# Performance work log

Hardware: AMD Instinct MI355X
Metric: run time of the kernel (lower is better)

Reference implementation:

```python
import jax, jax.numpy as jnp
import numpy as np

N = 4096
IN_DIM = 256
HID = 64
HEADS = 4
OUT_DIM = 64
NEG = -9e15


def setup_inputs() -> dict:
    key = jax.random.key(0)
    ks = jax.random.split(key, 12)
    h = jax.random.normal(ks[0], (N, IN_DIM), dtype=jnp.float32)
    adj = jax.random.randint(ks[1], (N, N), 0, 2, dtype=jnp.int32)
    # per-head GATLayer params (W: Linear(input_dim, hid) with bias; a: Linear(2*hid, 1) with bias)
    Wh = jax.random.normal(ks[2], (HEADS, IN_DIM, HID), dtype=jnp.float32) * (1.414 / np.sqrt(IN_DIM + HID))
    bWh = jnp.zeros((HEADS, HID), dtype=jnp.float32)
    a_src = jax.random.normal(ks[3], (HEADS, HID), dtype=jnp.float32) * 0.1
    a_dst = jax.random.normal(ks[4], (HEADS, HID), dtype=jnp.float32) * 0.1
    a_b = jnp.zeros((HEADS,), dtype=jnp.float32)
    # output GATLayer params
    Wo = jax.random.normal(ks[5], (HEADS * HID, OUT_DIM), dtype=jnp.float32) * (1.414 / np.sqrt(HEADS * HID + OUT_DIM))
    bWo = jnp.zeros((OUT_DIM,), dtype=jnp.float32)
    ao_src = jax.random.normal(ks[6], (OUT_DIM,), dtype=jnp.float32) * 0.1
    ao_dst = jax.random.normal(ks[7], (OUT_DIM,), dtype=jnp.float32) * 0.1
    ao_b = jnp.zeros((), dtype=jnp.float32)
    return {"h": h, "adj": adj, "Wh": Wh, "bWh": bWh, "a_src": a_src, "a_dst": a_dst,
            "a_b": a_b, "Wo": Wo, "bWo": bWo, "ao_src": ao_src, "ao_dst": ao_dst, "ao_b": ao_b}


def _gat_layer(x, adj_mask, W, b, a_s, a_d, a_bias):
    # x: [N, F], W: [F, D]. Decompose a([wh_i || wh_j]) = a_s.wh_i + a_d.wh_j + a_bias
    wh = x @ W + b                                   # [N, D]
    s = (wh @ a_s)[:, None] + (wh @ a_d)[None, :] + a_bias  # [N, N]
    s = jax.nn.leaky_relu(s, negative_slope=0.2)
    s = jnp.where(adj_mask, s, NEG)
    att = jax.nn.softmax(s, axis=1)                  # softmax over neighbors j
    return att @ wh                                  # [N, D]


def reference(h, adj, Wh, bWh, a_src, a_dst, a_b, Wo, bWo, ao_src, ao_dst, ao_b):
    adj_mask = adj > 0
    # multi-head: vmap over stacked head params (dropout is identity in eval)
    heads = jax.vmap(lambda W, b, asr, ads, ab: _gat_layer(h, adj_mask, W, b, asr, ads, ab))(
        Wh, bWh, a_src, a_dst, a_b)                  # [H, N, D]
    out = jax.nn.elu(heads)
    out = jnp.transpose(out, (1, 0, 2)).reshape(N, HEADS * HID)  # concat heads
    out = _gat_layer(out, adj_mask, Wo, bWo, ao_src, ao_dst, ao_b)
    return jax.nn.elu(out)
```

## Files before the change

### kernel.cpp

```cpp
#include <hip/hip_runtime.h>

#define NN 4096
#define NHEADS 4
#define HID 64
#define INDIM 256

using short8 = __attribute__((ext_vector_type(8))) short;
using f32x4  = __attribute__((ext_vector_type(4))) float;

union f32u { float f; unsigned int u; };

__device__ __forceinline__ float bf2f(unsigned short s) {
  f32u x; x.u = ((unsigned int)s) << 16; return x.f;
}
__device__ __forceinline__ unsigned short f2bf(float f) {
  f32u x; x.f = f;
  unsigned int r = x.u + 0x7fffu + ((x.u >> 16) & 1u);
  return (unsigned short)(r >> 16);
}

__device__ __forceinline__ float ld(const unsigned short* p, size_t i) { return bf2f(p[i]); }
__device__ __forceinline__ float ld(const float* p, size_t i) { return p[i]; }

__global__ __launch_bounds__(256) void k_probe(const void* hv, const void* adjv, int* flags) {
  __shared__ int s_bad, s_at;
  const int tid = threadIdx.x;
  if (tid == 0) { s_bad = 0; s_at = 0; }
  __syncthreads();
  const unsigned short* hu = (const unsigned short*)hv;
  float v = bf2f(hu[tid]);
  if (!(v > -1000.f && v < 1000.f)) atomicOr(&s_bad, 1);
  const unsigned int* au = (const unsigned int*)adjv;
  unsigned int wv = au[tid];
  if ((wv & 0xFFFFu) == 0x3F80u) atomicOr(&s_at, 2);
  else if (wv == 0x3F800000u) atomicOr(&s_at, 1);
  __syncthreads();
  if (tid == 0) {
    flags[0] = s_bad ? 0 : 1;
    int at = s_at;
    flags[1] = (at & 2) ? 2 : (at & 1);
  }
}

__global__ __launch_bounds__(256) void k_bm(const void* adjv, const int* __restrict__ flags,
                                            unsigned char* __restrict__ bm) {
  const int at = flags[1];
  const int i = blockIdx.x;
#pragma unroll
  for (int rep = 0; rep < 2; rep++) {
    int jb = threadIdx.x + rep * 256;
    unsigned int b = 0;
    if (at == 0) {
      const int4* arow = (const int4*)((const int*)adjv + (size_t)i * NN);
      int4 a0 = arow[jb * 2 + 0];
      int4 a1 = arow[jb * 2 + 1];
      b |= (a0.x > 0) ? 1u : 0u;  b |= (a0.y > 0) ? 2u : 0u;
      b |= (a0.z > 0) ? 4u : 0u;  b |= (a0.w > 0) ? 8u : 0u;
      b |= (a1.x > 0) ? 16u : 0u; b |= (a1.y > 0) ? 32u : 0u;
      b |= (a1.z > 0) ? 64u : 0u; b |= (a1.w > 0) ? 128u : 0u;
    } else if (at == 1) {
      const float* arow = (const float*)adjv + (size_t)i * NN + jb * 8;
      for (int t = 0; t < 8; t++) b |= (arow[t] > 0.5f) ? (1u << t) : 0u;
    } else {
      const unsigned short* arow = (const unsigned short*)adjv + (size_t)i * NN + jb * 8;
      for (int t = 0; t < 8; t++) b |= (bf2f(arow[t]) > 0.5f) ? (1u << t) : 0u;
    }
    bm[(size_t)i * 512 + jb] = (unsigned char)b;
  }
}

template <typename T>
__device__ __forceinline__ void wh_body(const T* h, const T* Wh, const T* bWh,
    const T* a_src, const T* a_dst, const T* a_b,
    unsigned short* Bp1, float* ssrc1, float* sdst1) {
  const int head = threadIdx.x >> 6;
  const int d = threadIdx.x & 63;
  const int i0 = blockIdx.x * 8;
  const T* W = Wh + (size_t)(head * INDIM) * HID + d;
  float acc[8];
  float bv = ld(bWh, head * HID + d);
#pragma unroll
  for (int r = 0; r < 8; r++) acc[r] = bv;
  for (int k = 0; k < INDIM; k++) {
    float wv = ld(W, (size_t)k * HID);
#pragma unroll
    for (int r = 0; r < 8; r++) {
      float hv = ld(h, (size_t)(i0 + r) * INDIM + k);
      acc[r] = fmaf(hv, wv, acc[r]);
    }
  }
  float asv = ld(a_src, head * HID + d);
  float adv = ld(a_dst, head * HID + d);
  float abv = ld(a_b, head);
#pragma unroll
  for (int r = 0; r < 8; r++) {
    float ps = acc[r] * asv, pd = acc[r] * adv;
#pragma unroll
    for (int o = 32; o > 0; o >>= 1) { ps += __shfl_xor(ps, o); pd += __shfl_xor(pd, o); }
    int i = i0 + r;
    if (d == 0) { ssrc1[head * NN + i] = ps + abv; sdst1[head * NN + i] = pd; }
    int kb = i >> 5, quad = (i >> 3) & 3, jj = i & 7;
    int ln = quad * 16 + (d & 15), tt = d >> 4;
    Bp1[((((size_t)head * 128 + kb) * 4 + tt) * 64 + ln) * 8 + jj] = f2bf(acc[r]);
  }
}
__global__ __launch_bounds__(256) void k_wh(const void* h, const void* Wh, const void* bWh,
    const void* a_src, const void* a_dst, const void* a_b, const int* __restrict__ flags,
    unsigned short* Bp1, float* ssrc1, float* sdst1) {
  if (flags[0])
    wh_body<unsigned short>((const unsigned short*)h, (const unsigned short*)Wh,
        (const unsigned short*)bWh, (const unsigned short*)a_src,
        (const unsigned short*)a_dst, (const unsigned short*)a_b, Bp1, ssrc1, sdst1);
  else
    wh_body<float>((const float*)h, (const float*)Wh, (const float*)bWh, (const float*)a_src,
        (const float*)a_dst, (const float*)a_b, Bp1, ssrc1, sdst1);
}

__global__ __launch_bounds__(1024) void k_att1(
    const unsigned char* __restrict__ bm, const float* __restrict__ ssrc,
    const float* __restrict__ sdst, const short8* __restrict__ Bp,
    unsigned short* __restrict__ x2) {
  const int rb = blockIdx.x;
  const int tid = threadIdx.x;
  const int w = tid >> 6;
  const int head = w & 3;
  const int slice = w >> 2;
  const int lane = tid & 63;
  const int r15 = lane & 15, quad = lane >> 4;
  const int row = rb * 16 + r15;
  const float si = ssrc[head * NN + row];
  const unsigned char* bmrow = bm + (size_t)row * 512;
  const float* sd = sdst + head * NN;
  const short8* Bh = Bp + (size_t)head * 128 * 4 * 64;
  f32x4 acc0 = {0, 0, 0, 0}, acc1 = {0, 0, 0, 0}, acc2 = {0, 0, 0, 0}, acc3 = {0, 0, 0, 0};
  float lsum = 0.f;
  const int kb0 = slice * 32;
  for (int kb = kb0; kb < kb0 + 32; kb++) {
    const int j0 = kb * 32 + quad * 8;
    unsigned int bits = bmrow[kb * 4 + quad];
    float4 q0 = *(const float4*)(sd + j0);
    float4 q1 = *(const float4*)(sd + j0 + 4);
    float sdv[8] = {q0.x, q0.y, q0.z, q0.w, q1.x, q1.y, q1.z, q1.w};
    short8 af;
#pragma unroll
    for (int jj = 0; jj < 8; jj++) {
      float t = si + sdv[jj];
      float lr = fmaxf(t, 0.2f * t);
      float e = __expf(lr);
      float pe = ((bits >> jj) & 1u) ? e : 0.0f;
      lsum += pe;
      af[jj] = (short)f2bf(pe);
    }
    const short8* Bk = Bh + (size_t)kb * 256 + lane;
    short8 b0 = Bk[0], b1 = Bk[64], b2 = Bk[128], b3 = Bk[192];
    acc0 = __builtin_amdgcn_mfma_f32_16x16x32_bf16(af, b0, acc0, 0, 0, 0);
    acc1 = __builtin_amdgcn_mfma_f32_16x16x32_bf16(af, b1, acc1, 0, 0, 0);
    acc2 = __builtin_amdgcn_mfma_f32_16x16x32_bf16(af, b2, acc2, 0, 0, 0);
    acc3 = __builtin_amdgcn_mfma_f32_16x16x32_bf16(af, b3, acc3, 0, 0, 0);
  }
  lsum += __shfl_xor(lsum, 16);
  lsum += __shfl_xor(lsum, 32);
  __shared__ float accs[8][16][66];
  __shared__ float ls[8][16];
  if (slice >= 2) {
    const int slot = w - 8;
    if (lane < 16) ls[slot][lane] = lsum;
#pragma unroll
    for (int g = 0; g < 4; g++) {
      int r = quad * 4 + g;
      accs[slot][r][ 0 + r15] = acc0[g];
      accs[slot][r][16 + r15] = acc1[g];
      accs[slot][r][32 + r15] = acc2[g];
      accs[slot][r][48 + r15] = acc3[g];
    }
  }
  __syncthreads();
  if (slice < 2) {
    const int slot = w;
    if (lane < 16) ls[slot][lane] += lsum;
#pragma unroll
    for (int g = 0; g < 4; g++) {
      int r = quad * 4 + g;
      accs[slot][r][ 0 + r15] += acc0[g];
      accs[slot][r][16 + r15] += acc1[g];
      accs[slot][r][32 + r15] += acc2[g];
      accs[slot][r][48 + r15] += acc3[g];
    }
  }
  __syncthreads();
#pragma unroll
  for (int c = tid; c < 4096; c += 1024) {
    int r = c >> 8, hc = c & 255;
    int hh = hc >> 6, col = hc & 63;
    float s = accs[hh][r][col] + accs[hh + 4][r][col];
    float lt = ls[hh][r] + ls[hh + 4][r];
    float v = (lt > 0.f) ? s / lt : 0.f;
    v = v > 0.f ? v : __expf(v) - 1.f;
    x2[(size_t)(rb * 16 + r) * 256 + hc] = f2bf(v);
  }
}

template <typename T>
__device__ __forceinline__ void wo_body(const unsigned short* x2, const T* Wo, const T* bWo,
    const T* ao_src, const T* ao_dst, const T* ao_b,
    unsigned short* Bp2, float* ssrc2, float* sdst2) {
  const int w = threadIdx.x >> 6, d = threadIdx.x & 63;
  const int i = blockIdx.x * 4 + w;
  const unsigned short* xr = x2 + (size_t)i * 256;
  float acc = ld(bWo, d);
  for (int k = 0; k < 256; k++)
    acc = fmaf(bf2f(xr[k]), ld(Wo, (size_t)k * 64 + d), acc);
  float ps = acc * ld(ao_src, d);
  float pd = acc * ld(ao_dst, d);
#pragma unroll
  for (int o = 32; o > 0; o >>= 1) { ps += __shfl_xor(ps, o); pd += __shfl_xor(pd, o); }
  if (d == 0) { ssrc2[i] = ps + ld(ao_b, 0); sdst2[i] = pd; }
  int kb = i >> 5, quad = (i >> 3) & 3, jj = i & 7;
  int ln = quad * 16 + (d & 15), tt = d >> 4;
  Bp2[(((size_t)kb * 4 + tt) * 64 + ln) * 8 + jj] = f2bf(acc);
}
__global__ __launch_bounds__(256) void k_wo(const unsigned short* __restrict__ x2,
    const void* Wo, const void* bWo, const void* ao_src, const void* ao_dst, const void* ao_b,
    const int* __restrict__ flags, unsigned short* Bp2, float* ssrc2, float* sdst2) {
  if (flags[0])
    wo_body<unsigned short>(x2, (const unsigned short*)Wo, (const unsigned short*)bWo,
        (const unsigned short*)ao_src, (const unsigned short*)ao_dst,
        (const unsigned short*)ao_b, Bp2, ssrc2, sdst2);
  else
    wo_body<float>(x2, (const float*)Wo, (const float*)bWo, (const float*)ao_src,
        (const float*)ao_dst, (const float*)ao_b, Bp2, ssrc2, sdst2);
}

__global__ __launch_bounds__(1024) void k_att2(
    const unsigned char* __restrict__ bm, const float* __restrict__ ssrc,
    const float* __restrict__ sdst, const short8* __restrict__ Bp,
    const int* __restrict__ flags, void* __restrict__ outv) {
  const int rb = blockIdx.x;
  const int tid = threadIdx.x;
  const int w = tid >> 6;
  const int lane = tid & 63;
  const int r15 = lane & 15, quad = lane >> 4;
  const int row = rb * 16 + r15;
  const float si = ssrc[row];
  const unsigned char* bmrow = bm + (size_t)row * 512;
  f32x4 acc0 = {0, 0, 0, 0}, acc1 = {0, 0, 0, 0}, acc2 = {0, 0, 0, 0}, acc3 = {0, 0, 0, 0};
  float lsum = 0.f;
  const int kb0 = w * 8;
  for (int kb = kb0; kb < kb0 + 8; kb++) {
    const int j0 = kb * 32 + quad * 8;
    unsigned int bits = bmrow[kb * 4 + quad];
    float4 q0 = *(const float4*)(sdst + j0);
    float4 q1 = *(const float4*)(sdst + j0 + 4);
    float sdv[8] = {q0.x, q0.y, q0.z, q0.w, q1.x, q1.y, q1.z, q1.w};
    short8 af;
#pragma unroll
    for (int jj = 0; jj < 8; jj++) {
      float t = si + sdv[jj];
      float lr = fmaxf(t, 0.2f * t);
      float e = __expf(lr);
      float pe = ((bits >> jj) & 1u) ? e : 0.0f;
      lsum += pe;
      af[jj] = (short)f2bf(pe);
    }
    const short8* Bk = Bp + (size_t)kb * 256 + lane;
    short8 b0 = Bk[0], b1 = Bk[64], b2 = Bk[128], b3 = Bk[192];
    acc0 = __builtin_amdgcn_mfma_f32_16x16x32_bf16(af, b0, acc0, 0, 0, 0);
    acc1 = __builtin_amdgcn_mfma_f32_16x16x32_bf16(af, b1, acc1, 0, 0, 0);
    acc2 = __builtin_amdgcn_mfma_f32_16x16x32_bf16(af, b2, acc2, 0, 0, 0);
    acc3 = __builtin_amdgcn_mfma_f32_16x16x32_bf16(af, b3, acc3, 0, 0, 0);
  }
  lsum += __shfl_xor(lsum, 16);
  lsum += __shfl_xor(lsum, 32);
  __shared__ float accs[8][16][66];
  __shared__ float ls2[8][16];
  if (w >= 8) {
    const int slot = w - 8;
    if (lane < 16) ls2[slot][lane] = lsum;
#pragma unroll
    for (int g = 0; g < 4; g++) {
      int r = quad * 4 + g;
      accs[slot][r][ 0 + r15] = acc0[g];
      accs[slot][r][16 + r15] = acc1[g];
      accs[slot][r][32 + r15] = acc2[g];
      accs[slot][r][48 + r15] = acc3[g];
    }
  }
  __syncthreads();
  if (w < 8) {
    const int slot = w;
    if (lane < 16) ls2[slot][lane] += lsum;
#pragma unroll
    for (int g = 0; g < 4; g++) {
      int r = quad * 4 + g;
      accs[slot][r][ 0 + r15] += acc0[g];
      accs[slot][r][16 + r15] += acc1[g];
      accs[slot][r][32 + r15] += acc2[g];
      accs[slot][r][48 + r15] += acc3[g];
    }
  }
  __syncthreads();
  {
    const int r = tid >> 6, col = tid & 63;
    float s = 0.f, lt = 0.f;
#pragma unroll
    for (int k = 0; k < 8; k++) { s += accs[k][r][col]; lt += ls2[k][r]; }
    float v = (lt > 0.f) ? s / lt : 0.f;
    v = v > 0.f ? v : __expf(v) - 1.f;
    size_t idx = (size_t)(rb * 16 + r) * 64 + col;
    if (flags[0]) ((unsigned short*)outv)[idx] = f2bf(v);
    else          ((float*)outv)[idx] = v;
  }
}

extern "C" void kernel_launch(void* const* d_in, const int* in_sizes, int n_in,
                              void* d_out, int out_size, void* d_ws, size_t ws_size,
                              hipStream_t stream) {
  const void* h      = d_in[0];
  const void* adj    = d_in[1];
  const void* Wh     = d_in[2];
  const void* bWh    = d_in[3];
  const void* a_src  = d_in[4];
  const void* a_dst  = d_in[5];
  const void* a_b    = d_in[6];
  const void* Wo     = d_in[7];
  const void* bWo    = d_in[8];
  const void* ao_src = d_in[9];
  const void* ao_dst = d_in[10];
  const void* ao_b   = d_in[11];

  size_t need = 16 + (size_t)NN * 512 + (size_t)NHEADS * NN * HID * 2 + (size_t)NN * 256 * 2 +
                (size_t)NN * 64 * 2 + (size_t)NHEADS * NN * 8 + (size_t)NN * 8;
  hipMemsetAsync(d_out, 0x41, (size_t)out_size * 2, stream);
  if (ws_size < need) {
    hipMemsetAsync(d_out, 0x45, (size_t)out_size * 2, stream);
    return;
  }
  unsigned char* ws = (unsigned char*)d_ws;
  int* flags = (int*)ws;                        ws += 16;
  unsigned char* bmp = ws;                      ws += (size_t)NN * 512;
  unsigned short* Bp1 = (unsigned short*)ws;    ws += (size_t)NHEADS * NN * HID * 2;
  unsigned short* x2  = (unsigned short*)ws;    ws += (size_t)NN * 256 * 2;
  unsigned short* Bp2 = (unsigned short*)ws;    ws += (size_t)NN * 64 * 2;
  float* ssrc1 = (float*)ws;                    ws += (size_t)NHEADS * NN * 4;
  float* sdst1 = (float*)ws;                    ws += (size_t)NHEADS * NN * 4;
  float* ssrc2 = (float*)ws;                    ws += (size_t)NN * 4;
  float* sdst2 = (float*)ws;                    ws += (size_t)NN * 4;

  k_probe<<<dim3(1),    dim3(256),  0, stream>>>(h, adj, flags);
  k_bm   <<<dim3(4096), dim3(256),  0, stream>>>(adj, flags, bmp);
  k_wh   <<<dim3(512),  dim3(256),  0, stream>>>(h, Wh, bWh, a_src, a_dst, a_b, flags,
                                                 Bp1, ssrc1, sdst1);
  k_att1 <<<dim3(256),  dim3(1024), 0, stream>>>(bmp, ssrc1, sdst1, (const short8*)Bp1, x2);
  k_wo   <<<dim3(1024), dim3(256),  0, stream>>>(x2, Wo, bWo, ao_src, ao_dst, ao_b, flags,
                                                 Bp2, ssrc2, sdst2);
  k_att2 <<<dim3(256),  dim3(1024), 0, stream>>>(bmp, ssrc2, sdst2, (const short8*)Bp2,
                                                 flags, d_out);
}
```

Baseline: 222.7 us.

## Split layer-1 attention into two-row-tile split-K kernel plus finalize pass

Adds k_att1s, in which each wave handles 32 rows (two 16-row tiles) so every B-fragment load feeds two MFMAs. The key dimension is split across two block halves, and the partial sums go to a workspace that a new finalize kernel (k_att1f) combines, normalises and passes through ELU. The adjacency bitmask is now read as int4 vectors, and float-to-bf16 packing uses the v_cvt_pk_bf16_f32 instruction in both attention kernels. This path only runs when the workspace is large enough, and it adds an extra kernel launch and fp32 partial-result traffic.

```diff
diff --git a/kernel.cpp b/kernel.cpp
--- a/kernel.cpp
+++ b/kernel.cpp
@@ -9,6 +9,7 @@
 using f32x4  = __attribute__((ext_vector_type(4))) float;
 
 union f32u { float f; unsigned int u; };
+union i4s8 { int4 i; short8 s; };
 
 __device__ __forceinline__ float bf2f(unsigned short s) {
   f32u x; x.u = ((unsigned int)s) << 16; return x.f;
@@ -17,6 +18,11 @@
   f32u x; x.f = f;
   unsigned int r = x.u + 0x7fffu + ((x.u >> 16) & 1u);
   return (unsigned short)(r >> 16);
+}
+__device__ __forceinline__ unsigned int cvtpk(float lo, float hi) {
+  unsigned int r;
+  asm("v_cvt_pk_bf16_f32 %0, %1, %2" : "=v"(r) : "v"(lo), "v"(hi));
+  return r;
 }
 
 __device__ __forceinline__ float ld(const unsigned short* p, size_t i) { return bf2f(p[i]); }
@@ -114,6 +120,129 @@
   else
     wh_body<float>((const float*)h, (const float*)Wh, (const float*)bWh, (const float*)a_src,
         (const float*)a_dst, (const float*)a_b, Bp1, ssrc1, sdst1);
+}
+
+__global__ __launch_bounds__(512, 6) void k_att1s(
+    const unsigned char* __restrict__ bm, const float* __restrict__ ssrc,
+    const float* __restrict__ sdst, const short8* __restrict__ Bp,
+    float* __restrict__ part, float* __restrict__ partl) {
+  const int rb = blockIdx.x & 127;
+  const int half = blockIdx.x >> 7;
+  const int tid = threadIdx.x;
+  const int w = tid >> 6;
+  const int head = w & 3;
+  const int sl = w >> 2;
+  const int lane = tid & 63;
+  const int r15 = lane & 15, quad = lane >> 4;
+  const int row0 = rb * 32 + r15;
+  const int row1 = row0 + 16;
+  const float si0 = ssrc[head * NN + row0];
+  const float si1 = ssrc[head * NN + row1];
+  const unsigned char* bmr0 = bm + (size_t)row0 * 512;
+  const unsigned char* bmr1 = bm + (size_t)row1 * 512;
+  const float* sd = sdst + head * NN;
+  const short8* Bh = Bp + (size_t)head * 128 * 4 * 64;
+  f32x4 acc0[4], acc1[4];
+#pragma unroll
+  for (int t = 0; t < 4; t++) { acc0[t] = (f32x4){0,0,0,0}; acc1[t] = (f32x4){0,0,0,0}; }
+  float ls0 = 0.f, ls1 = 0.f;
+  const int kb0 = half * 64 + sl * 32;
+  for (int g = 0; g < 8; g++) {
+    const int kbg = kb0 + g * 4;
+    int4 u0 = *(const int4*)(bmr0 + kbg * 4);
+    int4 u1 = *(const int4*)(bmr1 + kbg * 4);
+    int wd0[4] = {u0.x, u0.y, u0.z, u0.w};
+    int wd1[4] = {u1.x, u1.y, u1.z, u1.w};
+#pragma unroll
+    for (int kk = 0; kk < 4; kk++) {
+      const int kb = kbg + kk;
+      const int j0 = kb * 32 + quad * 8;
+      float4 q0 = *(const float4*)(sd + j0);
+      float4 q1 = *(const float4*)(sd + j0 + 4);
+      float sdv[8] = {q0.x, q0.y, q0.z, q0.w, q1.x, q1.y, q1.z, q1.w};
+      unsigned int bits0 = (((unsigned int)wd0[kk]) >> (quad * 8)) & 0xffu;
+      unsigned int bits1 = (((unsigned int)wd1[kk]) >> (quad * 8)) & 0xffu;
+      float pe0[8], pe1[8];
+#pragma unroll
+      for (int jj = 0; jj < 8; jj++) {
+        float t0 = si0 + sdv[jj];
+        float e0 = __expf(fmaxf(t0, 0.2f * t0));
+        pe0[jj] = ((bits0 >> jj) & 1u) ? e0 : 0.f;
+        ls0 += pe0[jj];
+        float t1 = si1 + sdv[jj];
+        float e1 = __expf(fmaxf(t1, 0.2f * t1));
+        pe1[jj] = ((bits1 >> jj) & 1u) ? e1 : 0.f;
+        ls1 += pe1[jj];
+      }
+      i4s8 a0, a1;
+      a0.i.x = cvtpk(pe0[0], pe0[1]); a0.i.y = cvtpk(pe0[2], pe0[3]);
+      a0.i.z = cvtpk(pe0[4], pe0[5]); a0.i.w = cvtpk(pe0[6], pe0[7]);
+      a1.i.x = cvtpk(pe1[0], pe1[1]); a1.i.y = cvtpk(pe1[2], pe1[3]);
+      a1.i.z = cvtpk(pe1[4], pe1[5]); a1.i.w = cvtpk(pe1[6], pe1[7]);
+      const short8* Bk = Bh + (size_t)kb * 256 + lane;
+      short8 bt[4];
+      bt[0] = Bk[0]; bt[1] = Bk[64]; bt[2] = Bk[128]; bt[3] = Bk[192];
+#pragma unroll
+      for (int t = 0; t < 4; t++) {
+        acc0[t] = __builtin_amdgcn_mfma_f32_16x16x32_bf16(a0.s, bt[t], acc0[t], 0, 0, 0);
+        acc1[t] = __builtin_amdgcn_mfma_f32_16x16x32_bf16(a1.s, bt[t], acc1[t], 0, 0, 0);
+      }
+    }
+  }
+  ls0 += __shfl_xor(ls0, 16); ls0 += __shfl_xor(ls0, 32);
+  ls1 += __shfl_xor(ls1, 16); ls1 += __shfl_xor(ls1, 32);
+  __shared__ float accs[4][16][66];
+  __shared__ float lsh[4][16];
+#define DOPASS(AC, LSV, PASS)                                                  \
+  do {                                                                         \
+    if (sl == 1) {                                                             \
+      if (lane < 16) lsh[head][lane] = (LSV);                                  \
+      _Pragma("unroll") for (int t = 0; t < 4; t++)                            \
+        _Pragma("unroll") for (int gg = 0; gg < 4; gg++)                       \
+          accs[head][quad * 4 + gg][t * 16 + r15] = (AC)[t][gg];               \
+    }                                                                          \
+    __syncthreads();                                                           \
+    if (sl == 0) {                                                             \
+      if (lane < 16) lsh[head][lane] += (LSV);                                 \
+      _Pragma("unroll") for (int t = 0; t < 4; t++)                            \
+        _Pragma("unroll") for (int gg = 0; gg < 4; gg++)                       \
+          accs[head][quad * 4 + gg][t * 16 + r15] += (AC)[t][gg];              \
+    }                                                                          \
+    __syncthreads();                                                           \
+    for (int idx = tid; idx < 4096; idx += 512) {                              \
+      int r = idx >> 8, hc = idx & 255;                                        \
+      part[((size_t)half * NN + rb * 32 + (PASS) * 16 + r) * 256 + hc] =       \
+          accs[hc >> 6][r][hc & 63];                                           \
+    }                                                                          \
+    if (tid < 64)                                                              \
+      partl[((size_t)half * 4 + (tid >> 4)) * NN + rb * 32 + (PASS) * 16 +     \
+            (tid & 15)] = lsh[tid >> 4][tid & 15];                             \
+    __syncthreads();                                                           \
+  } while (0)
+  DOPASS(acc0, ls0, 0);
+  DOPASS(acc1, ls1, 1);
+#undef DOPASS
+}
+
+__global__ __launch_bounds__(256) void k_att1f(const float* __restrict__ part,
+    const float* __restrict__ partl, unsigned short* __restrict__ x2) {
+  const int idx = blockIdx.x * 256 + threadIdx.x;
+  const int row = idx >> 6;
+  const int c4 = (idx & 63) * 4;
+  const int head = c4 >> 6;
+  const size_t off = (size_t)row * 256 + c4;
+  float4 p0 = *(const float4*)(part + off);
+  float4 p1 = *(const float4*)(part + (size_t)NN * 256 + off);
+  float lt = partl[(size_t)head * NN + row] + partl[(size_t)(4 + head) * NN + row];
+  float rl = (lt > 0.f) ? 1.f / lt : 0.f;
+  float v0 = (p0.x + p1.x) * rl, v1 = (p0.y + p1.y) * rl;
+  float v2 = (p0.z + p1.z) * rl, v3 = (p0.w + p1.w) * rl;
+  v0 = v0 > 0.f ? v0 : __expf(v0) - 1.f;
+  v1 = v1 > 0.f ? v1 : __expf(v1) - 1.f;
+  v2 = v2 > 0.f ? v2 : __expf(v2) - 1.f;
+  v3 = v3 > 0.f ? v3 : __expf(v3) - 1.f;
+  uint2 st; st.x = cvtpk(v0, v1); st.y = cvtpk(v2, v3);
+  *(uint2*)(x2 + off) = st;
 }
 
 __global__ __launch_bounds__(1024) void k_att1(
@@ -246,28 +375,36 @@
   f32x4 acc0 = {0, 0, 0, 0}, acc1 = {0, 0, 0, 0}, acc2 = {0, 0, 0, 0}, acc3 = {0, 0, 0, 0};
   float lsum = 0.f;
   const int kb0 = w * 8;
-  for (int kb = kb0; kb < kb0 + 8; kb++) {
-    const int j0 = kb * 32 + quad * 8;
-    unsigned int bits = bmrow[kb * 4 + quad];
-    float4 q0 = *(const float4*)(sdst + j0);
-    float4 q1 = *(const float4*)(sdst + j0 + 4);
-    float sdv[8] = {q0.x, q0.y, q0.z, q0.w, q1.x, q1.y, q1.z, q1.w};
-    short8 af;
-#pragma unroll
-    for (int jj = 0; jj < 8; jj++) {
-      float t = si + sdv[jj];
-      float lr = fmaxf(t, 0.2f * t);
-      float e = __expf(lr);
-      float pe = ((bits >> jj) & 1u) ? e : 0.0f;
-      lsum += pe;
-      af[jj] = (short)f2bf(pe);
-    }
-    const short8* Bk = Bp + (size_t)kb * 256 + lane;
-    short8 b0 = Bk[0], b1 = Bk[64], b2 = Bk[128], b3 = Bk[192];
-    acc0 = __builtin_amdgcn_mfma_f32_16x16x32_bf16(af, b0, acc0, 0, 0, 0);
-    acc1 = __builtin_amdgcn_mfma_f32_16x16x32_bf16(af, b1, acc1, 0, 0, 0);
-    acc2 = __builtin_amdgcn_mfma_f32_16x16x32_bf16(af, b2, acc2, 0, 0, 0);
-    acc3 = __builtin_amdgcn_mfma_f32_16x16x32_bf16(af, b3, acc3, 0, 0, 0);
+#pragma unroll
+  for (int g = 0; g < 2; g++) {
+    int4 ubm = *(const int4*)(bmrow + (kb0 + g * 4) * 4);
+    int wds[4] = {ubm.x, ubm.y, ubm.z, ubm.w};
+#pragma unroll
+    for (int kk = 0; kk < 4; kk++) {
+      const int kb = kb0 + g * 4 + kk;
+      const int j0 = kb * 32 + quad * 8;
+      unsigned int bits = (((unsigned int)wds[kk]) >> (quad * 8)) & 0xffu;
+      float4 q0 = *(const float4*)(sdst + j0);
+      float4 q1 = *(const float4*)(sdst + j0 + 4);
+      float sdv[8] = {q0.x, q0.y, q0.z, q0.w, q1.x, q1.y, q1.z, q1.w};
+      float pe[8];
+#pragma unroll
+      for (int jj = 0; jj < 8; jj++) {
+        float t = si + sdv[jj];
+        float e = __expf(fmaxf(t, 0.2f * t));
+        pe[jj] = ((bits >> jj) & 1u) ? e : 0.f;
+        lsum += pe[jj];
+      }
+      i4s8 a;
+      a.i.x = cvtpk(pe[0], pe[1]); a.i.y = cvtpk(pe[2], pe[3]);
+      a.i.z = cvtpk(pe[4], pe[5]); a.i.w = cvtpk(pe[6], pe[7]);
+      const short8* Bk = Bp + (size_t)kb * 256 + lane;
+      short8 b0 = Bk[0], b1 = Bk[64], b2 = Bk[128], b3 = Bk[192];
+      acc0 = __builtin_amdgcn_mfma_f32_16x16x32_bf16(a.s, b0, acc0, 0, 0, 0);
+      acc1 = __builtin_amdgcn_mfma_f32_16x16x32_bf16(a.s, b1, acc1, 0, 0, 0);
+      acc2 = __builtin_amdgcn_mfma_f32_16x16x32_bf16(a.s, b2, acc2, 0, 0, 0);
+      acc3 = __builtin_amdgcn_mfma_f32_16x16x32_bf16(a.s, b3, acc3, 0, 0, 0);
+    }
   }
   lsum += __shfl_xor(lsum, 16);
   lsum += __shfl_xor(lsum, 32);
@@ -328,13 +465,16 @@
   const void* ao_dst = d_in[10];
   const void* ao_b   = d_in[11];
 
-  size_t need = 16 + (size_t)NN * 512 + (size_t)NHEADS * NN * HID * 2 + (size_t)NN * 256 * 2 +
-                (size_t)NN * 64 * 2 + (size_t)NHEADS * NN * 8 + (size_t)NN * 8;
+  size_t need_old = 16 + (size_t)NN * 512 + (size_t)NHEADS * NN * HID * 2 +
+                    (size_t)NN * 256 * 2 + (size_t)NN * 64 * 2 +
+                    (size_t)NHEADS * NN * 8 + (size_t)NN * 8;
+  size_t need_new = need_old + (size_t)2 * NN * 256 * 4 + (size_t)2 * 4 * NN * 4;
   hipMemsetAsync(d_out, 0x41, (size_t)out_size * 2, stream);
-  if (ws_size < need) {
+  if (ws_size < need_old) {
     hipMemsetAsync(d_out, 0x45, (size_t)out_size * 2, stream);
     return;
   }
+  const bool big = ws_size >= need_new;
   unsigned char* ws = (unsigned char*)d_ws;
   int* flags = (int*)ws;                        ws += 16;
   unsigned char* bmp = ws;                      ws += (size_t)NN * 512;
@@ -345,12 +485,20 @@
   float* sdst1 = (float*)ws;                    ws += (size_t)NHEADS * NN * 4;
   float* ssrc2 = (float*)ws;                    ws += (size_t)NN * 4;
   float* sdst2 = (float*)ws;                    ws += (size_t)NN * 4;
+  float* part  = (float*)ws;                    ws += (size_t)2 * NN * 256 * 4;
+  float* partl = (float*)ws;                    ws += (size_t)2 * 4 * NN * 4;
 
   k_probe<<<dim3(1),    dim3(256),  0, stream>>>(h, adj, flags);
   k_bm   <<<dim3(4096), dim3(256),  0, stream>>>(adj, flags, bmp);
   k_wh   <<<dim3(512),  dim3(256),  0, stream>>>(h, Wh, bWh, a_src, a_dst, a_b, flags,
                                                  Bp1, ssrc1, sdst1);
-  k_att1 <<<dim3(256),  dim3(1024), 0, stream>>>(bmp, ssrc1, sdst1, (const short8*)Bp1, x2);
+  if (big) {
+    k_att1s<<<dim3(256),  dim3(512), 0, stream>>>(bmp, ssrc1, sdst1, (const short8*)Bp1,
+                                                  part, partl);
+    k_att1f<<<dim3(1024), dim3(256), 0, stream>>>(part, partl, x2);
+  } else {
+    k_att1<<<dim3(256), dim3(1024), 0, stream>>>(bmp, ssrc1, sdst1, (const short8*)Bp1, x2);
+  }
   k_wo   <<<dim3(1024), dim3(256),  0, stream>>>(x2, Wo, bWo, ao_src, ao_dst, ao_b, flags,
                                                  Bp2, ssrc2, sdst2);
   k_att2 <<<dim3(256),  dim3(1024), 0, stream>>>(bmp, ssrc2, sdst2, (const short8*)Bp2,
```

Result: slower. 304.6 us (+36.8%).
